# Kernel optimization log

Hardware: AMD Instinct MI355X
Metric: run time of the kernel (lower is better)

The kernel has to match this reference:

```python
import jax, jax.numpy as jnp
import numpy as np

Z_SIZE, H, EMB, C_FEAT, NMIX = 128, 512, 256, 512, 20


def setup_inputs() -> dict:
    key = jax.random.key(0)
    ks = jax.random.split(key, 20)
    B, T = 256, 256
    s = 0.02
    inp = {
        'backbone_feature': jax.random.normal(ks[0], (B, C_FEAT, 8, 8), jnp.float32),
        'z_vector': jax.random.normal(ks[1], (B, Z_SIZE), jnp.float32),
        'sketch_vector': jax.random.normal(ks[2], (T, B, 5), jnp.float32),
        'W_fc_hc': jax.random.normal(ks[3], (2 * H, Z_SIZE), jnp.float32) * s,
        'b_fc_hc': jnp.zeros((2 * H,), jnp.float32),
        'W_conv_h': jax.random.normal(ks[4], (EMB, H), jnp.float32) * s,
        'b_conv_h': jnp.zeros((EMB,), jnp.float32),
        'K_conv_f': jax.random.normal(ks[5], (EMB, C_FEAT, 3, 3), jnp.float32) * s,
        'b_conv_f': jnp.zeros((EMB,), jnp.float32),
        'W_conv_att': jax.random.normal(ks[6], (1, EMB), jnp.float32) * s,
        'b_conv_att': jnp.zeros((1,), jnp.float32),
        'W_ih': jax.random.normal(ks[7], (4 * H, H + 5), jnp.float32) * s,
        'W_hh': jax.random.normal(ks[8], (4 * H, H), jnp.float32) * s,
        'b_ih': jnp.zeros((4 * H,), jnp.float32),
        'b_hh': jnp.zeros((4 * H,), jnp.float32),
        'W_fc_params': jax.random.normal(ks[9], (6 * NMIX + 3, H), jnp.float32) * s,
        'b_fc_params': jnp.zeros((6 * NMIX + 3,), jnp.float32),
    }
    return inp


def _forward(backbone_feature, z_vector, sketch_vector,
             W_fc_hc, b_fc_hc, W_conv_h, b_conv_h, K_conv_f, b_conv_f,
             W_conv_att, b_conv_att, W_ih, W_hh, b_ih, b_hh,
             W_fc_params, b_fc_params):
    B = z_vector.shape[0]
    Hs, Ws = backbone_feature.shape[2], backbone_feature.shape[3]
    HW = Hs * Ws

    # initial hidden/cell from z
    hc = jnp.tanh(z_vector @ W_fc_hc.T + b_fc_hc)
    h0, c0 = hc[:, :H], hc[:, H:]

    # conv embedding of the feature map: unchanged across steps -> hoist
    x_em = jax.lax.conv_general_dilated(
        backbone_feature, K_conv_f, (1, 1), 'SAME',
        dimension_numbers=('NCHW', 'OIHW', 'NCHW')) + b_conv_f[None, :, None, None]
    x_em = x_em.reshape(B, EMB, HW).transpose(0, 2, 1)              # [B, HW, EMB]
    orgfeat = backbone_feature.reshape(B, C_FEAT, HW).transpose(0, 2, 1)  # [B, HW, C]

    start_token = jnp.tile(jnp.array([0., 0., 1., 0., 0.], jnp.float32), (B, 1))
    batch_init = jnp.concatenate([start_token[None], sketch_vector], axis=0)  # [T+1, B, 5]

    def step(carry, pt):
        h, c = carry
        g_em = h @ W_conv_h.T + b_conv_h                             # [B, EMB]
        feat = jnp.tanh(x_em + g_em[:, None, :])                     # [B, HW, EMB]
        score = feat @ W_conv_att.T + b_conv_att                     # [B, HW, 1]
        alpha = jax.nn.softmax(score, axis=1)
        att = jnp.sum(alpha * orgfeat, axis=1)                       # [B, C]
        x = jnp.concatenate([att, pt], axis=1)                       # [B, H+5]
        gates = x @ W_ih.T + h @ W_hh.T + b_ih + b_hh
        i, f, g, o = jnp.split(gates, 4, axis=1)
        c_new = jax.nn.sigmoid(f) * c + jax.nn.sigmoid(i) * jnp.tanh(g)
        h_new = jax.nn.sigmoid(o) * jnp.tanh(c_new)
        return (h_new, c_new), h_new

    _, hiddens = jax.lax.scan(step, (h0, c0), batch_init)            # [T+1, B, H]
    hiddens = hiddens.transpose(1, 0, 2)                             # [B, T+1, H]

    y = hiddens @ W_fc_params.T + b_fc_params                        # [B, T+1, 123]
    z_pen_logits = y[:, :, 0:3]
    z_pi, z_mu1, z_mu2, z_s1, z_s2, z_corr = jnp.split(y[:, :, 3:], 6, axis=2)
    z_pi = jax.nn.softmax(z_pi, axis=-1)
    z_s1, z_s2 = jnp.exp(z_s1), jnp.exp(z_s2)
    z_corr = jnp.tanh(z_corr)
    return (z_pi.reshape(-1, NMIX), z_mu1.reshape(-1, NMIX), z_mu2.reshape(-1, NMIX),
            z_s1.reshape(-1, NMIX), z_s2.reshape(-1, NMIX), z_corr.reshape(-1, NMIX),
            z_pen_logits.reshape(-1, 3))


def reference(backbone_feature, z_vector, sketch_vector,
              W_fc_hc, b_fc_hc, W_conv_h, b_conv_h, K_conv_f, b_conv_f,
              W_conv_att, b_conv_att, W_ih, W_hh, b_ih, b_hh,
              W_fc_params, b_fc_params):
    return _forward(backbone_feature, z_vector, sketch_vector,
                    W_fc_hc, b_fc_hc, W_conv_h, b_conv_h, K_conv_f, b_conv_f,
                    W_conv_att, b_conv_att, W_ih, W_hh, b_ih, b_hh,
                    W_fc_params, b_fc_params)
```

## Files before the change

### kernel.cpp

```cpp
#include <hip/hip_runtime.h>
#include <hip/hip_bf16.h>

typedef unsigned short u16;
typedef unsigned int   u32;
typedef unsigned long long u64;

typedef __attribute__((ext_vector_type(8))) short bf16x8;
typedef __attribute__((ext_vector_type(4))) float f32x4;
typedef __attribute__((ext_vector_type(4))) u32   u32x4;

#define L2E 1.44269504088896340736f

__device__ __forceinline__ float bf2f(u16 u){ union{u32 i; float f;} v; v.i=((u32)u)<<16; return v.f; }
__device__ __forceinline__ u16  f2bf(float f){ union{float f; u32 i;} v; v.f=f; u32 u=v.i; return (u16)((u + 0x7fffu + ((u>>16)&1u))>>16); }
__device__ __forceinline__ u32  packbf(float a,float b){ return (u32)f2bf(a) | ((u32)f2bf(b)<<16); }
__device__ __forceinline__ float tanh_f(float x){
  float cx = fminf(fmaxf(x,-15.f),15.f);
  float e  = __builtin_amdgcn_exp2f(cx*(2.f*L2E));
  return (e-1.f)*__builtin_amdgcn_rcpf(e+1.f);
}
__device__ __forceinline__ float sig_f(float x){
  float cx = fminf(fmaxf(x,-30.f),30.f);
  float e  = __builtin_amdgcn_exp2f(-cx*L2E);
  return __builtin_amdgcn_rcpf(1.f+e);
}
__device__ __forceinline__ u64   lda2(const u64* p){ return __hip_atomic_load((u64*)p, __ATOMIC_RELAXED, __HIP_MEMORY_SCOPE_AGENT); }
__device__ __forceinline__ u32   lda1(const u32* p){ return __hip_atomic_load((u32*)p, __ATOMIC_RELAXED, __HIP_MEMORY_SCOPE_AGENT); }
__device__ __forceinline__ void  sta(u32* p, u32 v){ __hip_atomic_store(p, v, __ATOMIC_RELAXED, __HIP_MEMORY_SCOPE_AGENT); }
__device__ __forceinline__ bf16x8 as_bf8(u32x4 w){ union{u32x4 u; bf16x8 b;} c; c.u=w; return c.b; }
__device__ __forceinline__ int frag_a(int r, int c){
  return ((c>>4)*2 + (r>>4))*256 + (((c>>2)&3))*64 + ((r&15))*4 + (c&3);
}

__device__ __forceinline__ void stage32i(u32* lds, const u32* gsrc, int t){
  const u64* g = (const u64*)gsrc;
  u64* d = (u64*)lds;
  u64 r[16];
  #pragma unroll
  for (int k=0;k<16;k++) r[k] = lda2(&g[k*256 + t]);
  #pragma unroll
  for (int k=0;k<16;k++) d[k*256 + t] = r[k];
}

__global__ void k_prep_w(const float* __restrict__ W_ih, const float* __restrict__ W_hh, u16* __restrict__ Wf){
  int idx = blockIdx.x*256 + threadIdx.x;
  int j    = idx & 7;
  int lane = (idx >> 3) & 63;
  int ks   = (idx >> 9) & 31;
  int nt   = (idx >> 14) & 3;
  int gs   = idx >> 16;
  int grow = nt*512 + gs*16 + (lane & 15);
  int k    = ks*32 + ((lane >> 4) & 3)*8 + j;
  float v = (k < 512) ? W_ih[grow*517 + k] : W_hh[grow*512 + (k - 512)];
  Wf[idx] = f2bf(v);
}
__global__ void k_prep_kf(const float* __restrict__ Kc, u16* __restrict__ Kf){
  int idx = blockIdx.x*256 + threadIdx.x;
  int j    = idx & 7;
  int lane = (idx >> 3) & 63;
  int ks   = (idx >> 9) & 15;
  int nt   = (idx >> 13) & 15;
  int tap  = idx >> 17;
  int oc = nt*16 + (lane & 15);
  int ic = ks*32 + ((lane >> 4) & 3)*8 + j;
  Kf[idx] = f2bf(Kc[(oc*512 + ic)*9 + tap]);
}
__global__ void k_prep_wcf2(const float* __restrict__ Wch, u16* __restrict__ WcF2){
  int idx = blockIdx.x*256 + threadIdx.x;
  int j = idx & 7, lane = (idx>>3) & 63, ks = (idx>>9) & 15, nt = idx >> 13;
  int e = nt*16 + (lane & 15);
  int k = ks*32 + ((lane >> 4) & 3)*8 + j;
  WcF2[idx] = f2bf(Wch[e*512 + k]);
}
__global__ void k_prep_wp(const float* __restrict__ Wp, u16* __restrict__ WpF){
  int idx = blockIdx.x*256 + threadIdx.x;
  int j = idx & 7, lane = (idx>>3) & 63, ks = (idx>>9) & 15, ntile = idx >> 13;
  int n = ntile*16 + (lane & 15);
  int k = ks*32 + (lane >> 4)*8 + j;
  WpF[idx] = (n < 123) ? f2bf(Wp[n*512 + k]) : (u16)0;
}
__global__ void k_hc(const float* __restrict__ z, const float* __restrict__ Wfc, const float* __restrict__ bfc,
                     u32* __restrict__ h_pack, float* __restrict__ c_ws){
  __shared__ float zl[128];
  int b = blockIdx.x, t = threadIdx.x;
  if (t < 128) zl[t] = z[b*128 + t];
  __syncthreads();
  float acc[4];
  #pragma unroll
  for (int i=0;i<4;i++){
    int n = 4*t + i;
    const float* row = Wfc + n*128;
    float a = 0.f;
    #pragma unroll 8
    for (int k2=0;k2<128;k2++) a += row[k2]*zl[k2];
    acc[i] = tanh_f(a + bfc[n]);
  }
  int bg = b >> 5, r = b & 31;
  if (t < 128){
    h_pack[bg*8192 + frag_a(r, 2*t)]   = packbf(acc[0], acc[1]);
    h_pack[bg*8192 + frag_a(r, 2*t+1)] = packbf(acc[2], acc[3]);
  } else {
    int base = 4*t - 512;
    #pragma unroll
    for (int i=0;i<4;i++) c_ws[b*512 + base + i] = acc[i];
  }
}
__device__ __forceinline__ int xt_addr(int p, int chunk){ return p*512 + ((chunk ^ (p & 7))<<3); }
__global__ __launch_bounds__(256) void k_conv(const float* __restrict__ bb, const u16* __restrict__ Kf,
                       const float* __restrict__ bcf, u16* __restrict__ x_em, u16* __restrict__ bb_bf){
  __shared__ u16 xt[64*512];
  int b = blockIdx.x, t = threadIdx.x;
  const float* src = bb + (size_t)b*512*64;
  u16* dstc = bb_bf + (size_t)b*512*64;
  for (int i=0;i<128;i++){
    int idx = i*256 + t;
    int ic = idx >> 6, p = idx & 63;
    u16 v = f2bf(src[idx]);
    xt[xt_addr(p, ic>>3) + (ic&7)] = v;
    dstc[idx] = v;
  }
  __syncthreads();
  int wv = t >> 6, l = t & 63, c0 = l & 15, q = l >> 4;
  f32x4 acc[4][4];
  #pragma unroll
  for (int a=0;a<4;a++)
    #pragma unroll
    for (int bq=0;bq<4;bq++) acc[a][bq] = (f32x4)0.f;
  for (int tap=0; tap<9; ++tap){
    int ty = tap/3 - 1, tx = tap%3 - 1;
    for (int ks=0; ks<16; ++ks){
      bf16x8 afr[4];
      #pragma unroll
      for (int mt=0; mt<4; ++mt){
        int p = mt*16 + c0;
        int py = (p >> 3) + ty, px = (p & 7) + tx;
        if ((unsigned)py < 8u && (unsigned)px < 8u){
          afr[mt] = *(const bf16x8*)(&xt[xt_addr(py*8+px, ks*4 + q)]);
        } else {
          afr[mt] = (bf16x8)0;
        }
      }
      #pragma unroll
      for (int ni=0; ni<4; ++ni){
        int nt = wv*4 + ni;
        bf16x8 bfr = as_bf8(*(const u32x4*)(const void*)(Kf + (size_t)((((tap*16 + nt)*16 + ks)*64) + l)*8));
        #pragma unroll
        for (int mt=0; mt<4; ++mt)
          acc[mt][ni] = __builtin_amdgcn_mfma_f32_16x16x32_bf16(afr[mt], bfr, acc[mt][ni], 0,0,0);
      }
    }
  }
  #pragma unroll
  for (int ni=0; ni<4; ++ni){
    int e = (wv*4+ni)*16 + c0;
    float bias = bcf[e];
    #pragma unroll
    for (int mt=0; mt<4; ++mt)
      #pragma unroll
      for (int r=0;r<4;r++){
        int p = mt*16 + q*4 + r;
        x_em[(size_t)(b*256 + e)*64 + p] = f2bf(acc[mt][ni][r] + bias);
      }
  }
}

__device__ __forceinline__ void bar_arrive(u32* flags, int bg, int gs, int t, u32 seq){
  __syncthreads();
  if (t == 0) sta(&flags[bg*64 + gs], seq);
}
__device__ __forceinline__ void bar_wait(u32* flags, int bg, int lane, u32 seq){
  const u32* f = &flags[bg*64 + (lane & 31)];
  for (;;){
    u32 v = lda1(f);
    if (__ballot(v < seq) == 0ull) break;
    __builtin_amdgcn_s_sleep(2);
  }
  __atomic_signal_fence(__ATOMIC_ACQUIRE);
}

__device__ __forceinline__ void head_post_par(const float* yL, const float* __restrict__ bp,
                                              float* __restrict__ out, float* mrsL,
                                              int gs, int bg, int t, int step){
  const int CH = 1315840;
  const int PEN = 7895040;
  if (gs == 0 && t < 32){
    float m = -1e30f;
    #pragma unroll 1
    for (int c=3;c<23;c++){ float v = yL[t*33 + c] + bp[c]; m = fmaxf(m, v); }
    float su = 0.f;
    #pragma unroll 1
    for (int c=3;c<23;c++){ float v = yL[t*33 + c] + bp[c]; su += __builtin_amdgcn_exp2f((v-m)*L2E); }
    mrsL[t*2]   = m;
    mrsL[t*2+1] = __builtin_amdgcn_rcpf(su);
  }
  __syncthreads();
  int b = t >> 3, cb = (t & 7)*4;
  float m = mrsL[b*2], rs = mrsL[b*2+1];
  int rr = (bg*32 + b)*257 + step;
  #pragma unroll
  for (int i=0;i<4;i++){
    int c2 = cb + i;
    int col = gs*32 + c2;
    if (col >= 123) break;
    float v = yL[b*33 + c2] + bp[col];
    float tv; int oidx;
    if (col < 3){ tv = v; oidx = PEN + rr*3 + col; }
    else {
      int j = col - 3, ch = j/20, jj = j - ch*20;
      if (ch == 0)      tv = __builtin_amdgcn_exp2f((v-m)*L2E)*rs;
      else if (ch <= 2) tv = v;
      else if (ch <= 4) tv = __builtin_amdgcn_exp2f(v*L2E);
      else              tv = tanh_f(v);
      oidx = ch*CH + rr*20 + jj;
    }
    __builtin_nontemporal_store(tv, &out[oidx]);
  }
}

__global__ __launch_bounds__(256) void k_rnn(
    const u16* __restrict__ bb_bf, const float* __restrict__ sketch,
    const float* __restrict__ b_ch, const float* __restrict__ Watt,
    const float* __restrict__ W_ih, const float* __restrict__ b_ih, const float* __restrict__ b_hh,
    const u16* __restrict__ x_em, const u16* __restrict__ Wf, const u16* __restrict__ WcF2,
    const u16* __restrict__ WpF, const float* __restrict__ bp,
    u32* __restrict__ h_pack, u32* __restrict__ att_pack,
    const float* __restrict__ c_ws, u32* __restrict__ flags, float* __restrict__ outp)
{
  __shared__ __align__(16) u32 hF[8192];
  __shared__ __align__(16) u32 attF[8192];
  __shared__ __align__(16) u32 xaH[4096];
  __shared__ __align__(16) u16 x_emL[16384];
  __shared__ float gemA[256];
  __shared__ float wattA[256];
  __shared__ float bchA[256];
  __shared__ float alphaL[64];
  __shared__ float ptL[32*8];
  __shared__ float w5L[64*8];
  __shared__ float biasL[64];
  __shared__ float yL[32*33];
  __shared__ float mrsL[64];
  float* gbufL = (float*)xaH;
  float* stgL  = (float*)xaH;

  int t = threadIdx.x;
  int bg = blockIdx.x >> 5, gs = blockIdx.x & 31;
  int lane = t & 63, wv = t >> 6;
  int c0 = lane & 15, q = lane >> 4;

  wattA[t] = Watt[t];
  bchA[t]  = b_ch[t];
  if (t < 64){
    int grow = (t >> 4)*512 + gs*16 + (t & 15);
    biasL[t] = b_ih[grow] + b_hh[grow];
    #pragma unroll
    for (int d=0; d<5; ++d) w5L[t*8+d] = W_ih[grow*517 + 512 + d];
  }
  int bL = t & 31, hp = t >> 5;
  int gb_l = bg*32 + bL;
  float c0r = c_ws[gb_l*512 + gs*16 + 2*hp];
  float c1r = c_ws[gb_l*512 + gs*16 + 2*hp + 1];
  int ba = bg*32 + gs;
  int mh_g = gs >> 4;
  int rq = (gs & 15) >> 2, rj = gs & 3;
  const u16* wb  = Wf   + (size_t)(((gs*4 + wv)*32)*64 + lane)*8;
  const u16* wcb = WcF2 + (size_t)((wv*4)*16*64 + lane)*8;
  const u32* hsrc = h_pack + (size_t)bg*8192;
  const u32* asrc = att_pack + (size_t)bg*8192;
  int hpub_a = frag_a(bL, gs*8 + hp);
  int apub_a = ((gs>>4)<<12) + ((t>>4)<<8) + (((t>>2)&3)<<6) + ((gs&15)<<2) + (t&3);
  {
    const u32x4* xs = (const u32x4*)(x_em + (size_t)ba*16384);
    u32x4* xd = (u32x4*)x_emL;
    #pragma unroll
    for (int i=0;i<8;i++) xd[i*256 + t] = xs[i*256 + t];
  }
  if (t < 32){
    ptL[t*8+0]=0.f; ptL[t*8+1]=0.f; ptL[t*8+2]=1.f; ptL[t*8+3]=0.f; ptL[t*8+4]=0.f;
  }
  u32 seq = 0;
  __syncthreads();

  #pragma clang loop unroll(disable)
  for (int ts=0; ts<257; ++ts){
    __syncthreads();
    stage32i(hF, hsrc, t);
    __syncthreads();
    {
      f32x4 ge0 = (f32x4)0.f, ge1 = (f32x4)0.f, ge2 = (f32x4)0.f, ge3 = (f32x4)0.f;
      #pragma unroll 8
      for (int ks=0; ks<16; ++ks){
        bf16x8 ahk = *(const bf16x8*)(&hF[(ks*2 + mh_g)*256 + lane*4]);
        bf16x8 b0 = as_bf8(*(const u32x4*)(const void*)(wcb + (size_t)(0*16 + ks)*512));
        bf16x8 b1 = as_bf8(*(const u32x4*)(const void*)(wcb + (size_t)(1*16 + ks)*512));
        bf16x8 b2 = as_bf8(*(const u32x4*)(const void*)(wcb + (size_t)(2*16 + ks)*512));
        bf16x8 b3 = as_bf8(*(const u32x4*)(const void*)(wcb + (size_t)(3*16 + ks)*512));
        ge0 = __builtin_amdgcn_mfma_f32_16x16x32_bf16(ahk, b0, ge0, 0,0,0);
        ge1 = __builtin_amdgcn_mfma_f32_16x16x32_bf16(ahk, b1, ge1, 0,0,0);
        ge2 = __builtin_amdgcn_mfma_f32_16x16x32_bf16(ahk, b2, ge2, 0,0,0);
        ge3 = __builtin_amdgcn_mfma_f32_16x16x32_bf16(ahk, b3, ge3, 0,0,0);
      }
      if (q == rq){
        gemA[(wv*4+0)*16 + c0] = ge0[rj] + bchA[(wv*4+0)*16 + c0];
        gemA[(wv*4+1)*16 + c0] = ge1[rj] + bchA[(wv*4+1)*16 + c0];
        gemA[(wv*4+2)*16 + c0] = ge2[rj] + bchA[(wv*4+2)*16 + c0];
        gemA[(wv*4+3)*16 + c0] = ge3[rj] + bchA[(wv*4+3)*16 + c0];
      }
    }
    __syncthreads();
    {
      int eg = t >> 3, ps = t & 7;
      float sp[8];
      #pragma unroll
      for (int j=0;j<8;j++) sp[j] = 0.f;
      const u16* xb = x_emL + (size_t)(eg*8)*64 + ps*8;
      #pragma unroll
      for (int e2=0; e2<8; ++e2){
        float gev = gemA[eg*8 + e2];
        float wev = wattA[eg*8 + e2];
        bf16x8 xv = *(const bf16x8*)(xb + (size_t)e2*64);
        #pragma unroll
        for (int j=0;j<8;j++)
          sp[j] += tanh_f(bf2f((u16)xv[j]) + gev) * wev;
      }
      #pragma unroll
      for (int j=0;j<8;j++) stgL[eg*64 + ps*8 + j] = sp[j];
    }
    __syncthreads();
    if (t < 64){
      float s = 0.f;
      #pragma unroll
      for (int g2=0; g2<32; ++g2) s += stgL[g2*64 + t];
      float m = s;
      #pragma unroll
      for (int d=1; d<64; d<<=1) m = fmaxf(m, __shfl_xor(m, d, 64));
      float ex = __builtin_amdgcn_exp2f((s - m) * L2E);
      float su = ex;
      #pragma unroll
      for (int d=1; d<64; d<<=1) su += __shfl_xor(su, d, 64);
      alphaL[t] = ex * __builtin_amdgcn_rcpf(su);
    }
    __syncthreads();
    {
      const u16* base = bb_bf + (size_t)(ba*512 + 2*t)*64;
      float a0 = 0.f, a1 = 0.f;
      #pragma unroll
      for (int p8=0; p8<8; ++p8){
        bf16x8 v0 = *(const bf16x8*)(base + p8*8);
        bf16x8 v1 = *(const bf16x8*)(base + 64 + p8*8);
        #pragma unroll
        for (int j=0;j<8;j++){
          float al = alphaL[p8*8+j];
          a0 += al * bf2f((u16)v0[j]);
          a1 += al * bf2f((u16)v1[j]);
        }
      }
      sta(&att_pack[(size_t)bg*8192 + apub_a], packbf(a0, a1));
    }
    seq++; bar_arrive(flags, bg, gs, t, seq);
    f32x4 acc0 = (f32x4)0.f, acc1 = (f32x4)0.f;
    #pragma unroll 8
    for (int ks2=0; ks2<16; ++ks2){
      bf16x8 bfr = as_bf8(*(const u32x4*)(const void*)(wb + (size_t)(16+ks2)*512));
      bf16x8 a0 = *(const bf16x8*)(&hF[(ks2*2)*256 + lane*4]);
      bf16x8 a1 = *(const bf16x8*)(&hF[(ks2*2+1)*256 + lane*4]);
      acc0 = __builtin_amdgcn_mfma_f32_16x16x32_bf16(a0, bfr, acc0, 0,0,0);
      acc1 = __builtin_amdgcn_mfma_f32_16x16x32_bf16(a1, bfr, acc1, 0,0,0);
    }
    bar_wait(flags, bg, lane, seq);
    stage32i(attF, asrc, t);
    __syncthreads();
    #pragma unroll 8
    for (int kc=0; kc<16; ++kc){
      bf16x8 bfr = as_bf8(*(const u32x4*)(const void*)(wb + (size_t)kc*512));
      bf16x8 af0 = *(const bf16x8*)(&attF[kc*256 + lane*4]);
      bf16x8 af1 = *(const bf16x8*)(&attF[4096 + kc*256 + lane*4]);
      acc0 = __builtin_amdgcn_mfma_f32_16x16x32_bf16(af0, bfr, acc0, 0,0,0);
      acc1 = __builtin_amdgcn_mfma_f32_16x16x32_bf16(af1, bfr, acc1, 0,0,0);
    }
    {
      int n = wv*16 + c0;
      #pragma unroll
      for (int r=0;r<4;r++){
        gbufL[n*33 + (q*4 + r)]      = acc0[r];
        gbufL[n*33 + (16 + q*4 + r)] = acc1[r];
      }
    }
    __syncthreads();
    {
      float p0v = ptL[bL*8+0], p1v = ptL[bL*8+1], p2v = ptL[bL*8+2], p3v = ptL[bL*8+3], p4v = ptL[bL*8+4];
      auto gval = [&](int n)->float {
        return gbufL[n*33 + bL] + biasL[n]
             + p0v*w5L[n*8+0] + p1v*w5L[n*8+1] + p2v*w5L[n*8+2] + p3v*w5L[n*8+3] + p4v*w5L[n*8+4];
      };
      float hv0 = 0.f, hv1 = 0.f;
      #pragma unroll
      for (int k2=0;k2<2;k2++){
        int hh = 2*hp + k2;
        float gi = gval(hh), gf = gval(16+hh), gg = gval(32+hh), go = gval(48+hh);
        float cp = k2 ? c1r : c0r;
        float cn = sig_f(gf)*cp + sig_f(gi)*tanh_f(gg);
        float hv = sig_f(go)*tanh_f(cn);
        if (k2){ c1r = cn; hv1 = hv; } else { c0r = cn; hv0 = hv; }
      }
      sta(&h_pack[(size_t)bg*8192 + hpub_a], packbf(hv0, hv1));
    }
    seq++; bar_arrive(flags, bg, gs, t, seq);
    if (ts < 256 && t < 32){
      const float* sp = sketch + ((size_t)ts*256 + (bg*32 + t))*5;
      ptL[t*8+0]=sp[0]; ptL[t*8+1]=sp[1]; ptL[t*8+2]=sp[2]; ptL[t*8+3]=sp[3]; ptL[t*8+4]=sp[4];
    }
    if (gs < 4 && ts > 0){
      int mh = wv & 1, nt2 = wv >> 1;
      f32x4 ya = (f32x4)0.f;
      #pragma unroll 8
      for (int ks=0; ks<16; ++ks){
        bf16x8 bw = as_bf8(*(const u32x4*)(const void*)(WpF + (size_t)((((gs*2+nt2)*16 + ks)*64) + lane)*8));
        bf16x8 ah = *(const bf16x8*)(&hF[(ks*2 + mh)*256 + lane*4]);
        ya = __builtin_amdgcn_mfma_f32_16x16x32_bf16(ah, bw, ya, 0,0,0);
      }
      #pragma unroll
      for (int r=0;r<4;r++) yL[(mh*16 + q*4 + r)*33 + nt2*16 + c0] = ya[r];
      __syncthreads();
      head_post_par(yL, bp, outp, mrsL, gs, bg, t, ts-1);
    }
    bar_wait(flags, bg, lane, seq);
  }
  if (gs < 4){
    __syncthreads();
    stage32i(hF, hsrc, t);
    __syncthreads();
    int mh = wv & 1, nt2 = wv >> 1;
    f32x4 ya = (f32x4)0.f;
    #pragma unroll 8
    for (int ks=0; ks<16; ++ks){
      bf16x8 bw = as_bf8(*(const u32x4*)(const void*)(WpF + (size_t)((((gs*2+nt2)*16 + ks)*64) + lane)*8));
      bf16x8 ah = *(const bf16x8*)(&hF[(ks*2 + mh)*256 + lane*4]);
      ya = __builtin_amdgcn_mfma_f32_16x16x32_bf16(ah, bw, ya, 0,0,0);
    }
    #pragma unroll
    for (int r=0;r<4;r++) yL[(mh*16 + q*4 + r)*33 + nt2*16 + c0] = ya[r];
    __syncthreads();
    head_post_par(yL, bp, outp, mrsL, gs, bg, t, 256);
  }
}

extern "C" void kernel_launch(void* const* d_in, const int* in_sizes, int n_in,
                              void* d_out, int out_size, void* d_ws, size_t ws_size,
                              hipStream_t stream){
  (void)in_sizes; (void)n_in; (void)out_size; (void)ws_size;
  const float* backbone = (const float*)d_in[0];
  const float* z_vec    = (const float*)d_in[1];
  const float* sketch   = (const float*)d_in[2];
  const float* W_fc_hc  = (const float*)d_in[3];
  const float* b_fc_hc  = (const float*)d_in[4];
  const float* W_conv_h = (const float*)d_in[5];
  const float* b_conv_h = (const float*)d_in[6];
  const float* K_conv_f = (const float*)d_in[7];
  const float* b_conv_f = (const float*)d_in[8];
  const float* W_att    = (const float*)d_in[9];
  const float* W_ih     = (const float*)d_in[11];
  const float* W_hh     = (const float*)d_in[12];
  const float* b_ih     = (const float*)d_in[13];
  const float* b_hh     = (const float*)d_in[14];
  const float* W_fcp    = (const float*)d_in[15];
  const float* b_fcp    = (const float*)d_in[16];

  char* ws = (char*)d_ws;
  u32*   flags    = (u32*)(ws + 0);
  u32*   h_pack   = (u32*)(ws + 16384);
  u32*   att_pack = (u32*)(ws + 278528);
  float* c_ws     = (float*)(ws + 2637824);
  u16*   x_em     = (u16*)(ws + 3162112);
  u16*   Wf       = (u16*)(ws + 11550720);
  u16*   Kf       = (u16*)(ws + 15745024);
  u16*   WcF2     = (u16*)(ws + 18104320);
  u16*   WpF      = (u16*)(ws + 18628608);
  u16*   bb_bf    = (u16*)(ws + 18759680);

  (void)hipMemsetAsync(flags, 0, 16384, stream);
  k_prep_w  <<<8192, 256, 0, stream>>>(W_ih, W_hh, Wf);
  k_prep_kf <<<4608, 256, 0, stream>>>(K_conv_f, Kf);
  k_prep_wcf2<<<512, 256, 0, stream>>>(W_conv_h, WcF2);
  k_prep_wp <<<256,  256, 0, stream>>>(W_fcp, WpF);
  k_hc      <<<256,  256, 0, stream>>>(z_vec, W_fc_hc, b_fc_hc, h_pack, c_ws);
  k_conv    <<<256,  256, 0, stream>>>(backbone, Kf, b_conv_f, x_em, bb_bf);
  k_rnn     <<<256,  256, 0, stream>>>(bb_bf, sketch, b_conv_h, W_att, W_ih, b_ih, b_hh,
                                       x_em, Wf, WcF2, WpF, b_fcp,
                                       h_pack, att_pack, c_ws, flags, (float*)d_out);
}
```

Before: 4.547 ms.

## Keep LSTM gate weight fragments resident in registers and poll barrier with one wave

Loads the per-wave W_ih/W_hh bf16 MFMA B-fragments (32 x bf16x8) into registers once before the 257-step loop instead of re-reading them from global memory every step. The cross-block barrier wait now has only the first wave poll the flags, with a longer sleep, and then releases the block with __syncthreads. Launch bounds are set to one block per CU so the compiler may use the extra VGPRs. This trades register pressure and possible spills for removing repeated weight loads from the serial recurrence, and cuts polling traffic.

```diff
diff --git a/kernel.cpp b/kernel.cpp
--- a/kernel.cpp
+++ b/kernel.cpp
@@ -168,14 +168,17 @@
   __syncthreads();
   if (t == 0) sta(&flags[bg*64 + gs], seq);
 }
-__device__ __forceinline__ void bar_wait(u32* flags, int bg, int lane, u32 seq){
-  const u32* f = &flags[bg*64 + (lane & 31)];
-  for (;;){
-    u32 v = lda1(f);
-    if (__ballot(v < seq) == 0ull) break;
-    __builtin_amdgcn_s_sleep(2);
+__device__ __forceinline__ void bar_wait(u32* flags, int bg, int t, u32 seq){
+  if (t < 32){
+    const u32* f = &flags[bg*64 + t];
+    for (;;){
+      u32 v = lda1(f);
+      if (__ballot(v < seq) == 0ull) break;
+      __builtin_amdgcn_s_sleep(4);
+    }
   }
   __atomic_signal_fence(__ATOMIC_ACQUIRE);
+  __syncthreads();
 }
 
 __device__ __forceinline__ void head_post_par(const float* yL, const float* __restrict__ bp,
@@ -217,7 +220,7 @@
   }
 }
 
-__global__ __launch_bounds__(256) void k_rnn(
+__global__ __launch_bounds__(256, 1) void k_rnn(
     const u16* __restrict__ bb_bf, const float* __restrict__ sketch,
     const float* __restrict__ b_ch, const float* __restrict__ Watt,
     const float* __restrict__ W_ih, const float* __restrict__ b_ih, const float* __restrict__ b_hh,
@@ -268,6 +271,12 @@
   const u32* asrc = att_pack + (size_t)bg*8192;
   int hpub_a = frag_a(bL, gs*8 + hp);
   int apub_a = ((gs>>4)<<12) + ((t>>4)<<8) + (((t>>2)&3)<<6) + ((gs&15)<<2) + (t&3);
+  bf16x8 wfA[16], wfH[16];
+  #pragma unroll
+  for (int k=0;k<16;k++){
+    wfA[k] = as_bf8(*(const u32x4*)(const void*)(wb + (size_t)k*512));
+    wfH[k] = as_bf8(*(const u32x4*)(const void*)(wb + (size_t)(16+k)*512));
+  }
   {
     const u32x4* xs = (const u32x4*)(x_em + (size_t)ba*16384);
     u32x4* xd = (u32x4*)x_emL;
@@ -358,24 +367,22 @@
     }
     seq++; bar_arrive(flags, bg, gs, t, seq);
     f32x4 acc0 = (f32x4)0.f, acc1 = (f32x4)0.f;
-    #pragma unroll 8
+    #pragma unroll
     for (int ks2=0; ks2<16; ++ks2){
-      bf16x8 bfr = as_bf8(*(const u32x4*)(const void*)(wb + (size_t)(16+ks2)*512));
       bf16x8 a0 = *(const bf16x8*)(&hF[(ks2*2)*256 + lane*4]);
       bf16x8 a1 = *(const bf16x8*)(&hF[(ks2*2+1)*256 + lane*4]);
-      acc0 = __builtin_amdgcn_mfma_f32_16x16x32_bf16(a0, bfr, acc0, 0,0,0);
-      acc1 = __builtin_amdgcn_mfma_f32_16x16x32_bf16(a1, bfr, acc1, 0,0,0);
-    }
-    bar_wait(flags, bg, lane, seq);
+      acc0 = __builtin_amdgcn_mfma_f32_16x16x32_bf16(a0, wfH[ks2], acc0, 0,0,0);
+      acc1 = __builtin_amdgcn_mfma_f32_16x16x32_bf16(a1, wfH[ks2], acc1, 0,0,0);
+    }
+    bar_wait(flags, bg, t, seq);
     stage32i(attF, asrc, t);
     __syncthreads();
-    #pragma unroll 8
+    #pragma unroll
     for (int kc=0; kc<16; ++kc){
-      bf16x8 bfr = as_bf8(*(const u32x4*)(const void*)(wb + (size_t)kc*512));
       bf16x8 af0 = *(const bf16x8*)(&attF[kc*256 + lane*4]);
       bf16x8 af1 = *(const bf16x8*)(&attF[4096 + kc*256 + lane*4]);
-      acc0 = __builtin_amdgcn_mfma_f32_16x16x32_bf16(af0, bfr, acc0, 0,0,0);
-      acc1 = __builtin_amdgcn_mfma_f32_16x16x32_bf16(af1, bfr, acc1, 0,0,0);
+      acc0 = __builtin_amdgcn_mfma_f32_16x16x32_bf16(af0, wfA[kc], acc0, 0,0,0);
+      acc1 = __builtin_amdgcn_mfma_f32_16x16x32_bf16(af1, wfA[kc], acc1, 0,0,0);
     }
     {
       int n = wv*16 + c0;
@@ -423,7 +430,7 @@
       __syncthreads();
       head_post_par(yL, bp, outp, mrsL, gs, bg, t, ts-1);
     }
-    bar_wait(flags, bg, lane, seq);
+    bar_wait(flags, bg, t, seq);
   }
   if (gs < 4){
     __syncthreads();
```

Result: no change. 4.594 ms (+1.0%).

## Merge pairs of RNN slice workgroups into 512-thread blocks to halve barrier participants

Applied to the files above, without the earlier changes.

The persistent RNN kernel now packs two gate-slice workgroups into one 512-thread block, each half keeping its own LDS buffers. The shared h/att staging into LDS is split across both halves, and the cross-block flag barrier waits on 16 blocks per batch group instead of 32. The aim is to cut inter-block synchronization and redundant global-to-LDS staging per timestep. The cost is more in-block __syncthreads coupling between the two halves and higher LDS use per block.

```diff
diff --git a/kernel.cpp b/kernel.cpp
--- a/kernel.cpp
+++ b/kernel.cpp
@@ -32,14 +32,14 @@
   return ((c>>4)*2 + (r>>4))*256 + (((c>>2)&3))*64 + ((r&15))*4 + (c&3);
 }
 
-__device__ __forceinline__ void stage32i(u32* lds, const u32* gsrc, int t){
+__device__ __forceinline__ void stage32h(u32* lds, const u32* gsrc, int t){
   const u64* g = (const u64*)gsrc;
   u64* d = (u64*)lds;
-  u64 r[16];
-  #pragma unroll
-  for (int k=0;k<16;k++) r[k] = lda2(&g[k*256 + t]);
-  #pragma unroll
-  for (int k=0;k<16;k++) d[k*256 + t] = r[k];
+  u64 r[8];
+  #pragma unroll
+  for (int k=0;k<8;k++) r[k] = lda2(&g[k*512 + t]);
+  #pragma unroll
+  for (int k=0;k<8;k++) d[k*512 + t] = r[k];
 }
 
 __global__ void k_prep_w(const float* __restrict__ W_ih, const float* __restrict__ W_hh, u16* __restrict__ Wf){
@@ -164,37 +164,36 @@
   }
 }
 
-__device__ __forceinline__ void bar_arrive(u32* flags, int bg, int gs, int t, u32 seq){
-  __syncthreads();
-  if (t == 0) sta(&flags[bg*64 + gs], seq);
-}
-__device__ __forceinline__ void bar_wait(u32* flags, int bg, int lane, u32 seq){
-  const u32* f = &flags[bg*64 + (lane & 31)];
-  for (;;){
-    u32 v = lda1(f);
-    if (__ballot(v < seq) == 0ull) break;
-    __builtin_amdgcn_s_sleep(2);
+__device__ __forceinline__ void bar_wait16(u32* flags, int bg, int t, u32 seq){
+  if (t < 64){
+    const u32* f = &flags[bg*64 + (t & 15)];
+    for (;;){
+      u32 v = lda1(f);
+      if (__ballot(v < seq) == 0ull) break;
+      __builtin_amdgcn_s_sleep(4);
+    }
   }
   __atomic_signal_fence(__ATOMIC_ACQUIRE);
+  __syncthreads();
 }
 
 __device__ __forceinline__ void head_post_par(const float* yL, const float* __restrict__ bp,
                                               float* __restrict__ out, float* mrsL,
-                                              int gs, int bg, int t, int step){
+                                              int gs, int bg, int th, int step){
   const int CH = 1315840;
   const int PEN = 7895040;
-  if (gs == 0 && t < 32){
+  if (gs == 0 && th < 32){
     float m = -1e30f;
     #pragma unroll 1
-    for (int c=3;c<23;c++){ float v = yL[t*33 + c] + bp[c]; m = fmaxf(m, v); }
+    for (int c=3;c<23;c++){ float v = yL[th*33 + c] + bp[c]; m = fmaxf(m, v); }
     float su = 0.f;
     #pragma unroll 1
-    for (int c=3;c<23;c++){ float v = yL[t*33 + c] + bp[c]; su += __builtin_amdgcn_exp2f((v-m)*L2E); }
-    mrsL[t*2]   = m;
-    mrsL[t*2+1] = __builtin_amdgcn_rcpf(su);
-  }
-  __syncthreads();
-  int b = t >> 3, cb = (t & 7)*4;
+    for (int c=3;c<23;c++){ float v = yL[th*33 + c] + bp[c]; su += __builtin_amdgcn_exp2f((v-m)*L2E); }
+    mrsL[th*2]   = m;
+    mrsL[th*2+1] = __builtin_amdgcn_rcpf(su);
+  }
+  __syncthreads();
+  int b = th >> 3, cb = (th & 7)*4;
   float m = mrsL[b*2], rs = mrsL[b*2+1];
   int rr = (bg*32 + b)*257 + step;
   #pragma unroll
@@ -216,8 +215,25 @@
     __builtin_nontemporal_store(tv, &out[oidx]);
   }
 }
-
-__global__ __launch_bounds__(256) void k_rnn(
+__device__ __forceinline__ void head_c(const u32* hF, const u16* __restrict__ WpF,
+                                       const float* __restrict__ bp, float* __restrict__ outp,
+                                       float* yL, float* mrsL, int gs, int bg, int t, int th, int step){
+  int lane = t & 63, wv = th >> 6, c0 = lane & 15, q = lane >> 4;
+  int mh = wv & 1, nt2 = wv >> 1;
+  f32x4 ya = (f32x4)0.f;
+  #pragma unroll 8
+  for (int ks=0; ks<16; ++ks){
+    bf16x8 bw = as_bf8(*(const u32x4*)(const void*)(WpF + (size_t)((((gs*2+nt2)*16 + ks)*64) + lane)*8));
+    bf16x8 ah = *(const bf16x8*)(&hF[(ks*2 + mh)*256 + lane*4]);
+    ya = __builtin_amdgcn_mfma_f32_16x16x32_bf16(ah, bw, ya, 0,0,0);
+  }
+  #pragma unroll
+  for (int r=0;r<4;r++) yL[(mh*16 + q*4 + r)*33 + nt2*16 + c0] = ya[r];
+  __syncthreads();
+  head_post_par(yL, bp, outp, mrsL, gs, bg, th, step);
+}
+
+__global__ __launch_bounds__(512, 1) void k_rnn(
     const u16* __restrict__ bb_bf, const float* __restrict__ sketch,
     const float* __restrict__ b_ch, const float* __restrict__ Watt,
     const float* __restrict__ W_ih, const float* __restrict__ b_ih, const float* __restrict__ b_hh,
@@ -228,37 +244,39 @@
 {
   __shared__ __align__(16) u32 hF[8192];
   __shared__ __align__(16) u32 attF[8192];
-  __shared__ __align__(16) u32 xaH[4096];
-  __shared__ __align__(16) u16 x_emL[16384];
-  __shared__ float gemA[256];
+  __shared__ __align__(16) u16 x_emL[2][16384];
+  __shared__ __align__(16) u32 xaH[2][2112];
+  __shared__ float gemA[2][256];
   __shared__ float wattA[256];
   __shared__ float bchA[256];
-  __shared__ float alphaL[64];
-  __shared__ float ptL[32*8];
-  __shared__ float w5L[64*8];
-  __shared__ float biasL[64];
-  __shared__ float yL[32*33];
-  __shared__ float mrsL[64];
-  float* gbufL = (float*)xaH;
-  float* stgL  = (float*)xaH;
+  __shared__ float alphaL[2][64];
+  __shared__ float ptL[2][256];
+  __shared__ float w5L[2][512];
+  __shared__ float biasL[2][64];
 
   int t = threadIdx.x;
-  int bg = blockIdx.x >> 5, gs = blockIdx.x & 31;
-  int lane = t & 63, wv = t >> 6;
+  int s  = t >> 8;
+  int th = t & 255;
+  int pr = blockIdx.x >> 4, gsp = blockIdx.x & 15;
+  int bg = pr;
+  int gs = gsp*2 + s;
+  int lane = t & 63, wv = th >> 6;
   int c0 = lane & 15, q = lane >> 4;
-
-  wattA[t] = Watt[t];
-  bchA[t]  = b_ch[t];
-  if (t < 64){
-    int grow = (t >> 4)*512 + gs*16 + (t & 15);
-    biasL[t] = b_ih[grow] + b_hh[grow];
+  float* stgL  = (float*)xaH[s];
+  float* gbufL = (float*)xaH[s];
+  float* yLs   = (float*)xaH[s];
+  float* mrsLs = (float*)xaH[s] + 1056;
+
+  if (t < 256){ wattA[t] = Watt[t]; bchA[t] = b_ch[t]; }
+  if (th < 64){
+    int grow = (th >> 4)*512 + gs*16 + (th & 15);
+    biasL[s][th] = b_ih[grow] + b_hh[grow];
     #pragma unroll
-    for (int d=0; d<5; ++d) w5L[t*8+d] = W_ih[grow*517 + 512 + d];
-  }
-  int bL = t & 31, hp = t >> 5;
-  int gb_l = bg*32 + bL;
-  float c0r = c_ws[gb_l*512 + gs*16 + 2*hp];
-  float c1r = c_ws[gb_l*512 + gs*16 + 2*hp + 1];
+    for (int d=0; d<5; ++d) w5L[s][th*8+d] = W_ih[grow*517 + 512 + d];
+  }
+  int bL = th & 31, hp = th >> 5;
+  float c0r = c_ws[(bg*32 + bL)*512 + gs*16 + 2*hp];
+  float c1r = c_ws[(bg*32 + bL)*512 + gs*16 + 2*hp + 1];
   int ba = bg*32 + gs;
   int mh_g = gs >> 4;
   int rq = (gs & 15) >> 2, rj = gs & 3;
@@ -267,15 +285,17 @@
   const u32* hsrc = h_pack + (size_t)bg*8192;
   const u32* asrc = att_pack + (size_t)bg*8192;
   int hpub_a = frag_a(bL, gs*8 + hp);
-  int apub_a = ((gs>>4)<<12) + ((t>>4)<<8) + (((t>>2)&3)<<6) + ((gs&15)<<2) + (t&3);
+  int apub_a = ((gs>>4)<<12) + ((th>>4)<<8) + (((th>>2)&3)<<6) + ((gs&15)<<2) + (th&3);
+  u32* hpub = h_pack + (size_t)bg*8192 + hpub_a;
+  u32* apub = att_pack + (size_t)bg*8192 + apub_a;
   {
     const u32x4* xs = (const u32x4*)(x_em + (size_t)ba*16384);
-    u32x4* xd = (u32x4*)x_emL;
+    u32x4* xd = (u32x4*)x_emL[s];
     #pragma unroll
-    for (int i=0;i<8;i++) xd[i*256 + t] = xs[i*256 + t];
-  }
-  if (t < 32){
-    ptL[t*8+0]=0.f; ptL[t*8+1]=0.f; ptL[t*8+2]=1.f; ptL[t*8+3]=0.f; ptL[t*8+4]=0.f;
+    for (int i=0;i<8;i++) xd[i*256 + th] = xs[i*256 + th];
+  }
+  if (th < 32){
+    ptL[s][th*8+0]=0.f; ptL[s][th*8+1]=0.f; ptL[s][th*8+2]=1.f; ptL[s][th*8+3]=0.f; ptL[s][th*8+4]=0.f;
   }
   u32 seq = 0;
   __syncthreads();
@@ -283,39 +303,39 @@
   #pragma clang loop unroll(disable)
   for (int ts=0; ts<257; ++ts){
     __syncthreads();
-    stage32i(hF, hsrc, t);
+    stage32h(hF, hsrc, t);
     __syncthreads();
     {
-      f32x4 ge0 = (f32x4)0.f, ge1 = (f32x4)0.f, ge2 = (f32x4)0.f, ge3 = (f32x4)0.f;
+      f32x4 e0=(f32x4)0.f, e1=(f32x4)0.f, e2=(f32x4)0.f, e3=(f32x4)0.f;
       #pragma unroll 8
       for (int ks=0; ks<16; ++ks){
-        bf16x8 ahk = *(const bf16x8*)(&hF[(ks*2 + mh_g)*256 + lane*4]);
+        bf16x8 hk = *(const bf16x8*)(&hF[(ks*2 + mh_g)*256 + lane*4]);
         bf16x8 b0 = as_bf8(*(const u32x4*)(const void*)(wcb + (size_t)(0*16 + ks)*512));
         bf16x8 b1 = as_bf8(*(const u32x4*)(const void*)(wcb + (size_t)(1*16 + ks)*512));
         bf16x8 b2 = as_bf8(*(const u32x4*)(const void*)(wcb + (size_t)(2*16 + ks)*512));
         bf16x8 b3 = as_bf8(*(const u32x4*)(const void*)(wcb + (size_t)(3*16 + ks)*512));
-        ge0 = __builtin_amdgcn_mfma_f32_16x16x32_bf16(ahk, b0, ge0, 0,0,0);
-        ge1 = __builtin_amdgcn_mfma_f32_16x16x32_bf16(ahk, b1, ge1, 0,0,0);
-        ge2 = __builtin_amdgcn_mfma_f32_16x16x32_bf16(ahk, b2, ge2, 0,0,0);
-        ge3 = __builtin_amdgcn_mfma_f32_16x16x32_bf16(ahk, b3, ge3, 0,0,0);
+        e0 = __builtin_amdgcn_mfma_f32_16x16x32_bf16(hk, b0, e0, 0,0,0);
+        e1 = __builtin_amdgcn_mfma_f32_16x16x32_bf16(hk, b1, e1, 0,0,0);
+        e2 = __builtin_amdgcn_mfma_f32_16x16x32_bf16(hk, b2, e2, 0,0,0);
+        e3 = __builtin_amdgcn_mfma_f32_16x16x32_bf16(hk, b3, e3, 0,0,0);
       }
       if (q == rq){
-        gemA[(wv*4+0)*16 + c0] = ge0[rj] + bchA[(wv*4+0)*16 + c0];
-        gemA[(wv*4+1)*16 + c0] = ge1[rj] + bchA[(wv*4+1)*16 + c0];
-        gemA[(wv*4+2)*16 + c0] = ge2[rj] + bchA[(wv*4+2)*16 + c0];
-        gemA[(wv*4+3)*16 + c0] = ge3[rj] + bchA[(wv*4+3)*16 + c0];
+        gemA[s][(wv*4+0)*16 + c0] = e0[rj] + bchA[(wv*4+0)*16 + c0];
+        gemA[s][(wv*4+1)*16 + c0] = e1[rj] + bchA[(wv*4+1)*16 + c0];
+        gemA[s][(wv*4+2)*16 + c0] = e2[rj] + bchA[(wv*4+2)*16 + c0];
+        gemA[s][(wv*4+3)*16 + c0] = e3[rj] + bchA[(wv*4+3)*16 + c0];
       }
     }
     __syncthreads();
     {
-      int eg = t >> 3, ps = t & 7;
+      int eg = th >> 3, ps = th & 7;
       float sp[8];
       #pragma unroll
       for (int j=0;j<8;j++) sp[j] = 0.f;
-      const u16* xb = x_emL + (size_t)(eg*8)*64 + ps*8;
+      const u16* xb = x_emL[s] + (size_t)(eg*8)*64 + ps*8;
       #pragma unroll
       for (int e2=0; e2<8; ++e2){
-        float gev = gemA[eg*8 + e2];
+        float gev = gemA[s][eg*8 + e2];
         float wev = wattA[eg*8 + e2];
         bf16x8 xv = *(const bf16x8*)(xb + (size_t)e2*64);
         #pragma unroll
@@ -326,22 +346,22 @@
       for (int j=0;j<8;j++) stgL[eg*64 + ps*8 + j] = sp[j];
     }
     __syncthreads();
-    if (t < 64){
-      float s = 0.f;
-      #pragma unroll
-      for (int g2=0; g2<32; ++g2) s += stgL[g2*64 + t];
-      float m = s;
+    if (th < 64){
+      float sv = 0.f;
+      #pragma unroll
+      for (int g2=0; g2<32; ++g2) sv += stgL[g2*64 + th];
+      float m = sv;
       #pragma unroll
       for (int d=1; d<64; d<<=1) m = fmaxf(m, __shfl_xor(m, d, 64));
-      float ex = __builtin_amdgcn_exp2f((s - m) * L2E);
+      float ex = __builtin_amdgcn_exp2f((sv - m) * L2E);
       float su = ex;
       #pragma unroll
       for (int d=1; d<64; d<<=1) su += __shfl_xor(su, d, 64);
-      alphaL[t] = ex * __builtin_amdgcn_rcpf(su);
+      alphaL[s][th] = ex * __builtin_amdgcn_rcpf(su);
     }
     __syncthreads();
     {
-      const u16* base = bb_bf + (size_t)(ba*512 + 2*t)*64;
+      const u16* base = bb_bf + (size_t)(ba*512 + 2*th)*64;
       float a0 = 0.f, a1 = 0.f;
       #pragma unroll
       for (int p8=0; p8<8; ++p8){
@@ -349,14 +369,16 @@
         bf16x8 v1 = *(const bf16x8*)(base + 64 + p8*8);
         #pragma unroll
         for (int j=0;j<8;j++){
-          float al = alphaL[p8*8+j];
+          float al = alphaL[s][p8*8+j];
           a0 += al * bf2f((u16)v0[j]);
           a1 += al * bf2f((u16)v1[j]);
         }
       }
-      sta(&att_pack[(size_t)bg*8192 + apub_a], packbf(a0, a1));
-    }
-    seq++; bar_arrive(flags, bg, gs, t, seq);
+      sta(apub, packbf(a0, a1));
+    }
+    seq++;
+    __syncthreads();
+    if (t == 0) sta(&flags[bg*64 + gsp], seq);
     f32x4 acc0 = (f32x4)0.f, acc1 = (f32x4)0.f;
     #pragma unroll 8
     for (int ks2=0; ks2<16; ++ks2){
@@ -366,8 +388,8 @@
       acc0 = __builtin_amdgcn_mfma_f32_16x16x32_bf16(a0, bfr, acc0, 0,0,0);
       acc1 = __builtin_amdgcn_mfma_f32_16x16x32_bf16(a1, bfr, acc1, 0,0,0);
     }
-    bar_wait(flags, bg, lane, seq);
-    stage32i(attF, asrc, t);
+    bar_wait16(flags, bg, t, seq);
+    stage32h(attF, asrc, t);
     __syncthreads();
     #pragma unroll 8
     for (int kc=0; kc<16; ++kc){
@@ -387,10 +409,11 @@
     }
     __syncthreads();
     {
-      float p0v = ptL[bL*8+0], p1v = ptL[bL*8+1], p2v = ptL[bL*8+2], p3v = ptL[bL*8+3], p4v = ptL[bL*8+4];
+      const float* pl = ptL[s];
+      float p0v = pl[bL*8+0], p1v = pl[bL*8+1], p2v = pl[bL*8+2], p3v = pl[bL*8+3], p4v = pl[bL*8+4];
       auto gval = [&](int n)->float {
-        return gbufL[n*33 + bL] + biasL[n]
-             + p0v*w5L[n*8+0] + p1v*w5L[n*8+1] + p2v*w5L[n*8+2] + p3v*w5L[n*8+3] + p4v*w5L[n*8+4];
+        return gbufL[n*33 + bL] + biasL[s][n]
+             + p0v*w5L[s][n*8+0] + p1v*w5L[s][n*8+1] + p2v*w5L[s][n*8+2] + p3v*w5L[s][n*8+3] + p4v*w5L[s][n*8+4];
       };
       float hv0 = 0.f, hv1 = 0.f;
       #pragma unroll
@@ -402,45 +425,26 @@
         float hv = sig_f(go)*tanh_f(cn);
         if (k2){ c1r = cn; hv1 = hv; } else { c0r = cn; hv0 = hv; }
       }
-      sta(&h_pack[(size_t)bg*8192 + hpub_a], packbf(hv0, hv1));
-    }
-    seq++; bar_arrive(flags, bg, gs, t, seq);
-    if (ts < 256 && t < 32){
-      const float* sp = sketch + ((size_t)ts*256 + (bg*32 + t))*5;
-      ptL[t*8+0]=sp[0]; ptL[t*8+1]=sp[1]; ptL[t*8+2]=sp[2]; ptL[t*8+3]=sp[3]; ptL[t*8+4]=sp[4];
-    }
-    if (gs < 4 && ts > 0){
-      int mh = wv & 1, nt2 = wv >> 1;
-      f32x4 ya = (f32x4)0.f;
-      #pragma unroll 8
-      for (int ks=0; ks<16; ++ks){
-        bf16x8 bw = as_bf8(*(const u32x4*)(const void*)(WpF + (size_t)((((gs*2+nt2)*16 + ks)*64) + lane)*8));
-        bf16x8 ah = *(const bf16x8*)(&hF[(ks*2 + mh)*256 + lane*4]);
-        ya = __builtin_amdgcn_mfma_f32_16x16x32_bf16(ah, bw, ya, 0,0,0);
-      }
-      #pragma unroll
-      for (int r=0;r<4;r++) yL[(mh*16 + q*4 + r)*33 + nt2*16 + c0] = ya[r];
-      __syncthreads();
-      head_post_par(yL, bp, outp, mrsL, gs, bg, t, ts-1);
-    }
-    bar_wait(flags, bg, lane, seq);
-  }
-  if (gs < 4){
-    __syncthreads();
-    stage32i(hF, hsrc, t);
-    __syncthreads();
-    int mh = wv & 1, nt2 = wv >> 1;
-    f32x4 ya = (f32x4)0.f;
-    #pragma unroll 8
-    for (int ks=0; ks<16; ++ks){
-      bf16x8 bw = as_bf8(*(const u32x4*)(const void*)(WpF + (size_t)((((gs*2+nt2)*16 + ks)*64) + lane)*8));
-      bf16x8 ah = *(const bf16x8*)(&hF[(ks*2 + mh)*256 + lane*4]);
-      ya = __builtin_amdgcn_mfma_f32_16x16x32_bf16(ah, bw, ya, 0,0,0);
-    }
-    #pragma unroll
-    for (int r=0;r<4;r++) yL[(mh*16 + q*4 + r)*33 + nt2*16 + c0] = ya[r];
-    __syncthreads();
-    head_post_par(yL, bp, outp, mrsL, gs, bg, t, 256);
+      sta(hpub, packbf(hv0, hv1));
+    }
+    seq++;
+    __syncthreads();
+    if (t == 0) sta(&flags[bg*64 + gsp], seq);
+    if (ts < 256 && th < 32){
+      const float* sp2 = sketch + ((size_t)ts*256 + bg*32 + th)*5;
+      float* pl = ptL[s];
+      pl[th*8+0]=sp2[0]; pl[th*8+1]=sp2[1]; pl[th*8+2]=sp2[2]; pl[th*8+3]=sp2[3]; pl[th*8+4]=sp2[4];
+    }
+    if (gsp < 2 && ts > 0){
+      head_c(hF, WpF, bp, outp, yLs, mrsLs, gs, bg, t, th, ts-1);
+    }
+    bar_wait16(flags, bg, t, seq);
+  }
+  if (gsp < 2){
+    __syncthreads();
+    stage32h(hF, hsrc, t);
+    __syncthreads();
+    head_c(hF, WpF, bp, outp, yLs, mrsLs, gs, bg, t, th, 256);
   }
 }
 
@@ -484,7 +488,7 @@
   k_prep_wp <<<256,  256, 0, stream>>>(W_fcp, WpF);
   k_hc      <<<256,  256, 0, stream>>>(z_vec, W_fc_hc, b_fc_hc, h_pack, c_ws);
   k_conv    <<<256,  256, 0, stream>>>(backbone, Kf, b_conv_f, x_em, bb_bf);
-  k_rnn     <<<256,  256, 0, stream>>>(bb_bf, sketch, b_conv_h, W_att, W_ih, b_ih, b_hh,
+  k_rnn     <<<128,  512, 0, stream>>>(bb_bf, sketch, b_conv_h, W_att, W_ih, b_ih, b_hh,
                                        x_em, Wf, WcF2, WpF, b_fcp,
                                        h_pack, att_pack, c_ws, flags, (float*)d_out);
 }
```

Measured after the change: 10.93 ms. 140% more time.
